# Performance work log

Measured on AMD Instinct MI355X. Metric: run time of the kernel, lower is better.

## Reference

```python
import jax, jax.numpy as jnp
import numpy as np

# tiny-cuda-nn canonical 2D image hash-grid config
L = 16            # n_levels
F = 2             # n_features_per_level
T = 1 << 19       # hashmap size per level
BASE = 16         # base_resolution
SCALE = 1.5       # per_level_scale
HIDDEN = 64
ENC_DIM = L * F   # 32
OUT = 3           # rgb
S = 1024          # img_res / output_size
PRIME_Y = np.uint32(2654435761)


def setup_inputs() -> dict:
    key = jax.random.key(0)
    k1, k2, k3, k4 = jax.random.split(key, 4)
    # pixel-center grid exactly as in the torch module
    half = 0.5 / S
    xs = jnp.linspace(half, 1.0 - half, S, dtype=jnp.float32)
    xv, yv = jnp.meshgrid(xs, xs, indexing='ij')
    xy = jnp.stack([yv.flatten(), xv.flatten()], axis=1)  # [S*S, 2]
    # tcnn initializes hash tables ~ U(-1e-4, 1e-4)
    hash_tables = jax.random.uniform(k1, (L, T, F), jnp.float32, -1e-4, 1e-4)
    W0 = jax.random.normal(k2, (ENC_DIM, HIDDEN), jnp.float32) * np.sqrt(2.0 / ENC_DIM)
    W1 = jax.random.normal(k3, (HIDDEN, HIDDEN), jnp.float32) * np.sqrt(2.0 / HIDDEN)
    W2 = jax.random.normal(k4, (HIDDEN, OUT), jnp.float32) * np.sqrt(2.0 / HIDDEN)
    return {"xy": xy, "hash_tables": hash_tables, "W0": W0, "W1": W1, "W2": W2}


def _encode(xy, hash_tables):
    # multiresolution hash-grid encoding with bilinear interpolation
    resolutions = jnp.floor(BASE * SCALE ** jnp.arange(L)).astype(jnp.int32)  # [L]
    offs = jnp.array([[0, 0], [0, 1], [1, 0], [1, 1]], jnp.int32)            # [4,2]

    def level(table, res):
        pos = xy * res.astype(xy.dtype)            # [N,2]
        p0 = jnp.floor(pos).astype(jnp.int32)
        w = pos - p0                                # frac weights [N,2]
        corners = p0[:, None, :] + offs[None]       # [N,4,2]
        # hashed index (tcnn spatial hash): x*1 ^ y*PRIME, mod T
        cu = corners.astype(jnp.uint32)
        hidx = ((cu[..., 0] ^ (cu[..., 1] * PRIME_Y)) % np.uint32(T)).astype(jnp.int32)
        # dense index when the grid fits in the table
        didx = corners[..., 0] + corners[..., 1] * (res + 1)
        idx = jnp.where((res + 1) * (res + 1) <= T, didx, hidx)  # [N,4]
        f = table[idx]                               # [N,4,F] gather
        wx, wy = w[:, 0:1], w[:, 1:2]
        wts = jnp.stack([(1 - wx) * (1 - wy), (1 - wx) * wy,
                         wx * (1 - wy), wx * wy], axis=1)  # [N,4,1]
        return jnp.sum(f * wts, axis=1)              # [N,F]

    feats = jax.vmap(level, in_axes=(0, 0), out_axes=1)(hash_tables, resolutions)  # [N,L,F]
    return feats.reshape(feats.shape[0], ENC_DIM)


def reference(xy, hash_tables, W0, W1, W2):
    enc = _encode(xy, hash_tables)                  # [N,32]
    h = jax.nn.relu(enc @ W0)                       # tiny MLP, no bias (FullyFusedMLP)
    h = jax.nn.relu(h @ W1)
    out = h @ W2                                    # [N,3], linear output
    return out.reshape(S, S, OUT).transpose(2, 0, 1)  # [3,S,S]
```

## Files before the change

### kernel.cpp

```cpp
#include <hip/hip_runtime.h>
#include <cstdint>
#include <cstddef>

#define S_DIM 1024
#define NPTS (S_DIM * S_DIM)
#define NLEV 16
#define TBL (1u << 19)
#define TMASK (TBL - 1u)
#define PRIME_Y 2654435761u

typedef float v4f __attribute__((ext_vector_type(4)));
typedef short v8s __attribute__((ext_vector_type(8)));

__device__ __forceinline__ void split2(float a, float b, uint32_t& hi, uint32_t& lo) {
    uint32_t ua = __float_as_uint(a), ub = __float_as_uint(b);
    uint32_t ha = ua & 0xFFFF0000u, hb = ub & 0xFFFF0000u;
    float la = a - __uint_as_float(ha);
    float lb = b - __uint_as_float(hb);
    hi = (ha >> 16) | hb;
    lo = (__float_as_uint(la) >> 16) | (__float_as_uint(lb) & 0xFFFF0000u);
}

__global__ __launch_bounds__(256) void prep_weights(const float* __restrict__ W0,
                                                    const float* __restrict__ W1,
                                                    uint4* __restrict__ ws) {
    const int tid = threadIdx.x;
    const int lane = tid & 63;
    const int m = lane & 15, q = lane >> 4;

    {
        const int tile = tid >> 6;
        const int n = tile * 16 + m;
        uint32_t hi[4], lo[4];
        #pragma unroll
        for (int d = 0; d < 4; ++d) {
            const int k0 = q * 8 + 2 * d;
            split2(W0[k0 * 64 + n], W0[(k0 + 1) * 64 + n], hi[d], lo[d]);
        }
        ws[tid]       = make_uint4(hi[0], hi[1], hi[2], hi[3]);
        ws[256 + tid] = make_uint4(lo[0], lo[1], lo[2], lo[3]);
    }

    #pragma unroll
    for (int rep = 0; rep < 2; ++rep) {
        const int unit = tid + rep * 256;
        const int l2 = unit & 63, frag = unit >> 6;
        const int nt = frag >> 1, ks = frag & 1;
        const int mm = l2 & 15, qq = l2 >> 4;
        const int n = nt * 16 + mm;
        uint32_t hi[4], lo[4];
        #pragma unroll
        for (int d = 0; d < 4; ++d) {
            const int k0 = ks * 32 + qq * 8 + 2 * d;
            split2(W1[k0 * 64 + n], W1[(k0 + 1) * 64 + n], hi[d], lo[d]);
        }
        ws[512 + unit]  = make_uint4(hi[0], hi[1], hi[2], hi[3]);
        ws[1024 + unit] = make_uint4(lo[0], lo[1], lo[2], lo[3]);
    }
}

static __device__ __forceinline__ float2 level_feat_rt(float x, float y, float fr,
                                                       int st , bool dense,
                                                       const float* __restrict__ tb) {
    const float px = x * fr, py = y * fr;
    const float fx = floorf(px), fy = floorf(py);
    const float wx = px - fx, wy = py - fy;
    const int x0 = (int)fx, y0 = (int)fy;

    const int d00 = x0 + y0 * st;
    const int d01 = d00 + st;
    const unsigned a = (unsigned)x0, b = (unsigned)y0;
    const unsigned hb0 = b * PRIME_Y;
    const unsigned hb1 = hb0 + PRIME_Y;
    const int h00 = (int)((a ^ hb0) & TMASK);
    const int h01 = (int)((a ^ hb1) & TMASK);
    const int h10 = (int)(((a + 1u) ^ hb0) & TMASK);
    const int h11 = (int)(((a + 1u) ^ hb1) & TMASK);

    const int i00 = dense ? d00 : h00;
    const int i01 = dense ? d01 : h01;
    const int i10 = dense ? (d00 + 1) : h10;
    const int i11 = dense ? (d01 + 1) : h11;

    const float2 f00 = *(const float2*)(tb + 2 * (size_t)i00);
    const float2 f01 = *(const float2*)(tb + 2 * (size_t)i01);
    const float2 f10 = *(const float2*)(tb + 2 * (size_t)i10);
    const float2 f11 = *(const float2*)(tb + 2 * (size_t)i11);

    const float omx = 1.f - wx, omy = 1.f - wy;
    const float w00 = omx * omy, w01 = omx * wy, w10 = wx * omy, w11 = wx * wy;

    float2 e;
    e.x = f00.x * w00 + f01.x * w01 + f10.x * w10 + f11.x * w11;
    e.y = f00.y * w00 + f01.y * w01 + f10.y * w10 + f11.y * w11;
    return e;
}

__global__ __launch_bounds__(256, 2) void ngp_mfma(
    const float* __restrict__ xy,
    const float* __restrict__ tables,
    const float* __restrict__ W2,
    const uint4* __restrict__ ws,
    float* __restrict__ out)
{
    __shared__ uint4 w1LDS[1024];
    __shared__ alignas(16) uint32_t h0LDS[4 * 16 * 68];
    __shared__ alignas(16) float w2t[3 * 64];

    const int tid = threadIdx.x;
    const int lane = tid & 63;
    const int wave = tid >> 6;
    const int m = lane & 15, q = lane >> 4;
    const int blockBase = blockIdx.x * 256;
    const int pbase = blockBase + wave * 64 + m;

    #pragma unroll
    for (int r = 0; r < 4; ++r) w1LDS[r * 256 + tid] = ws[512 + r * 256 + tid];
    if (tid < 192) w2t[(tid % 3) * 64 + (tid / 3)] = W2[tid];

    v8s w0h[4], w0l[4];
    #pragma unroll
    for (int t4 = 0; t4 < 4; ++t4) {
        w0h[t4] = __builtin_bit_cast(v8s, ws[t4 * 64 + lane]);
        w0l[t4] = __builtin_bit_cast(v8s, ws[256 + t4 * 64 + lane]);
    }

    constexpr float RESF[NLEV] = {16.f, 24.f, 36.f, 54.f, 81.f, 121.f, 182.f, 273.f,
                                  410.f, 615.f, 922.f, 1383.f, 2075.f, 3113.f, 4670.f, 7006.f};
#define LVLF(i) ((q & 2) ? ((q & 1) ? RESF[12 + (i)] : RESF[8 + (i)]) \
                         : ((q & 1) ? RESF[4 + (i)]  : RESF[(i)]))
    const float fr0 = LVLF(0), fr1 = LVLF(1), fr2 = LVLF(2), fr3 = LVLF(3);
#undef LVLF
    const int st0 = (int)fr0 + 1, st1 = (int)fr1 + 1;
    const int st2 = (int)fr2 + 1, st3 = (int)fr3 + 1;
    const bool dn0 = (q <= 2), dn1 = (q <= 2), dn2 = (q <= 1), dn3 = (q <= 1);
    const float* tb0 = tables + ((size_t)(unsigned)(q * 4 + 0) << 20);
    const float* tb1 = tables + ((size_t)(unsigned)(q * 4 + 1) << 20);
    const float* tb2 = tables + ((size_t)(unsigned)(q * 4 + 2) << 20);
    const float* tb3 = tables + ((size_t)(unsigned)(q * 4 + 3) << 20);

    __syncthreads();

    #pragma unroll 1
    for (int t = 0; t < 4; ++t) {
        const float2 p = ((const float2*)xy)[pbase + t * 16];
        const float2 e0 = level_feat_rt(p.x, p.y, fr0, st0, dn0, tb0);
        const float2 e1 = level_feat_rt(p.x, p.y, fr1, st1, dn1, tb1);
        const float2 e2 = level_feat_rt(p.x, p.y, fr2, st2, dn2, tb2);
        const float2 e3 = level_feat_rt(p.x, p.y, fr3, st3, dn3, tb3);
        uint32_t eh0, el0, eh1, el1, eh2, el2, eh3, el3;
        split2(e0.x, e0.y, eh0, el0);
        split2(e1.x, e1.y, eh1, el1);
        split2(e2.x, e2.y, eh2, el2);
        split2(e3.x, e3.y, eh3, el3);
        const v8s eH = __builtin_bit_cast(v8s, make_uint4(eh0, eh1, eh2, eh3));
        const v8s eL = __builtin_bit_cast(v8s, make_uint4(el0, el1, el2, el3));

        v4f acc0[4];
        #pragma unroll
        for (int nt = 0; nt < 4; ++nt) {
            v4f c = {0.f, 0.f, 0.f, 0.f};
            c = __builtin_amdgcn_mfma_f32_16x16x32_bf16(w0l[nt], eH, c, 0, 0, 0);
            c = __builtin_amdgcn_mfma_f32_16x16x32_bf16(w0h[nt], eL, c, 0, 0, 0);
            c = __builtin_amdgcn_mfma_f32_16x16x32_bf16(w0h[nt], eH, c, 0, 0, 0);
            acc0[nt] = c;
        }

        uint32_t* hrow = h0LDS + (wave * 16 + m) * 68;
        #pragma unroll
        for (int nt = 0; nt < 4; ++nt) {
            const float r0 = fmaxf(acc0[nt][0], 0.f), r1 = fmaxf(acc0[nt][1], 0.f);
            const float r2 = fmaxf(acc0[nt][2], 0.f), r3 = fmaxf(acc0[nt][3], 0.f);
            uint32_t h0w, l0w, h1w, l1w;
            split2(r0, r1, h0w, l0w);
            split2(r2, r3, h1w, l1w);
            *((uint2*)(hrow + nt * 8 + q * 2))      = make_uint2(h0w, h1w);
            *((uint2*)(hrow + 32 + nt * 8 + q * 2)) = make_uint2(l0w, l1w);
        }

        const v8s b0H = __builtin_bit_cast(v8s, *((const uint4*)(hrow + q * 4)));
        const v8s b0L = __builtin_bit_cast(v8s, *((const uint4*)(hrow + 32 + q * 4)));
        const v8s b1H = __builtin_bit_cast(v8s, *((const uint4*)(hrow + 16 + q * 4)));
        const v8s b1L = __builtin_bit_cast(v8s, *((const uint4*)(hrow + 48 + q * 4)));

        float o0 = 0.f, o1 = 0.f, o2 = 0.f;
        #pragma unroll
        for (int nt = 0; nt < 4; ++nt) {
            const v8s a0h = __builtin_bit_cast(v8s, w1LDS[(nt * 2 + 0) * 64 + lane]);
            const v8s a0l = __builtin_bit_cast(v8s, w1LDS[512 + (nt * 2 + 0) * 64 + lane]);
            const v8s a1h = __builtin_bit_cast(v8s, w1LDS[(nt * 2 + 1) * 64 + lane]);
            const v8s a1l = __builtin_bit_cast(v8s, w1LDS[512 + (nt * 2 + 1) * 64 + lane]);
            v4f c = {0.f, 0.f, 0.f, 0.f};
            c = __builtin_amdgcn_mfma_f32_16x16x32_bf16(a0l, b0H, c, 0, 0, 0);
            c = __builtin_amdgcn_mfma_f32_16x16x32_bf16(a0h, b0L, c, 0, 0, 0);
            c = __builtin_amdgcn_mfma_f32_16x16x32_bf16(a0h, b0H, c, 0, 0, 0);
            c = __builtin_amdgcn_mfma_f32_16x16x32_bf16(a1l, b1H, c, 0, 0, 0);
            c = __builtin_amdgcn_mfma_f32_16x16x32_bf16(a1h, b1L, c, 0, 0, 0);
            c = __builtin_amdgcn_mfma_f32_16x16x32_bf16(a1h, b1H, c, 0, 0, 0);

            const int n = nt * 16 + q * 4;
            const float4 wa = *((const float4*)(w2t + 0 * 64 + n));
            const float4 wb = *((const float4*)(w2t + 1 * 64 + n));
            const float4 wc = *((const float4*)(w2t + 2 * 64 + n));
            const float h0r = fmaxf(c[0], 0.f), h1r = fmaxf(c[1], 0.f);
            const float h2r = fmaxf(c[2], 0.f), h3r = fmaxf(c[3], 0.f);
            o0 = fmaf(h0r, wa.x, fmaf(h1r, wa.y, fmaf(h2r, wa.z, fmaf(h3r, wa.w, o0))));
            o1 = fmaf(h0r, wb.x, fmaf(h1r, wb.y, fmaf(h2r, wb.z, fmaf(h3r, wb.w, o1))));
            o2 = fmaf(h0r, wc.x, fmaf(h1r, wc.y, fmaf(h2r, wc.z, fmaf(h3r, wc.w, o2))));
        }

        o0 += __shfl_xor(o0, 16); o0 += __shfl_xor(o0, 32);
        o1 += __shfl_xor(o1, 16); o1 += __shfl_xor(o1, 32);
        o2 += __shfl_xor(o2, 16); o2 += __shfl_xor(o2, 32);

        if (lane < 16) {
            const int pidx = blockBase + wave * 64 + t * 16 + lane;
            out[pidx] = o0;
            out[NPTS + pidx] = o1;
            out[2 * NPTS + pidx] = o2;
        }
    }
}

extern "C" void kernel_launch(void* const* d_in, const int* in_sizes, int n_in,
                              void* d_out, int out_size, void* d_ws, size_t ws_size,
                              hipStream_t stream) {
    const float* xy     = (const float*)d_in[0];
    const float* tables = (const float*)d_in[1];
    const float* W0     = (const float*)d_in[2];
    const float* W1     = (const float*)d_in[3];
    const float* W2     = (const float*)d_in[4];
    float* out = (float*)d_out;
    uint4* ws  = (uint4*)d_ws;

    hipLaunchKernelGGL(prep_weights, dim3(1), dim3(256), 0, stream, W0, W1, ws);
    hipLaunchKernelGGL(ngp_mfma, dim3(NPTS / 256), dim3(256), 0, stream,
                       xy, tables, W2, ws, out);
}
```

Baseline: 186.5 us.

## Software-pipeline hash-table gathers one tile ahead of the MLP compute

Splits the level lookup into an issue phase (index computation and gathers) and an interpolation phase. The gathers for the next 16-point tile are issued before the current tile's MFMA work, and the first tile's gathers are issued before the weight staging into LDS, so gather latency can hide behind compute. The bilinear interpolation also moves to packed 2-wide FMAs. In exchange, about 40 extra VGPRs hold the in-flight gather results, which may press occupancy at launch bounds of 256 threads with 2 blocks.

```diff
diff --git a/kernel.cpp b/kernel.cpp
--- a/kernel.cpp
+++ b/kernel.cpp
@@ -9,8 +9,14 @@
 #define TMASK (TBL - 1u)
 #define PRIME_Y 2654435761u
 
+typedef float v2f __attribute__((ext_vector_type(2)));
 typedef float v4f __attribute__((ext_vector_type(4)));
 typedef short v8s __attribute__((ext_vector_type(8)));
+
+static __device__ __forceinline__ v2f fma2(v2f a, v2f b, v2f c) {
+    return __builtin_elementwise_fma(a, b, c);
+}
+static __device__ __forceinline__ v2f splat2(float s) { return (v2f){s, s}; }
 
 __device__ __forceinline__ void split2(float a, float b, uint32_t& hi, uint32_t& lo) {
     uint32_t ua = __float_as_uint(a), ub = __float_as_uint(b);
@@ -59,40 +65,36 @@
     }
 }
 
-static __device__ __forceinline__ float2 level_feat_rt(float x, float y, float fr,
-                                                       int st , bool dense,
-                                                       const float* __restrict__ tb) {
+static __device__ __forceinline__ void level_issue(
+    float x, float y, float fr, int st, bool dense, const float* __restrict__ tb,
+    v2f& w, v2f& f00, v2f& f01, v2f& f10, v2f& f11)
+{
     const float px = x * fr, py = y * fr;
     const float fx = floorf(px), fy = floorf(py);
-    const float wx = px - fx, wy = py - fy;
+    w = (v2f){px - fx, py - fy};
     const int x0 = (int)fx, y0 = (int)fy;
 
     const int d00 = x0 + y0 * st;
-    const int d01 = d00 + st;
     const unsigned a = (unsigned)x0, b = (unsigned)y0;
-    const unsigned hb0 = b * PRIME_Y;
-    const unsigned hb1 = hb0 + PRIME_Y;
-    const int h00 = (int)((a ^ hb0) & TMASK);
-    const int h01 = (int)((a ^ hb1) & TMASK);
-    const int h10 = (int)(((a + 1u) ^ hb0) & TMASK);
-    const int h11 = (int)(((a + 1u) ^ hb1) & TMASK);
-
-    const int i00 = dense ? d00 : h00;
-    const int i01 = dense ? d01 : h01;
-    const int i10 = dense ? (d00 + 1) : h10;
-    const int i11 = dense ? (d01 + 1) : h11;
-
-    const float2 f00 = *(const float2*)(tb + 2 * (size_t)i00);
-    const float2 f01 = *(const float2*)(tb + 2 * (size_t)i01);
-    const float2 f10 = *(const float2*)(tb + 2 * (size_t)i10);
-    const float2 f11 = *(const float2*)(tb + 2 * (size_t)i11);
-
-    const float omx = 1.f - wx, omy = 1.f - wy;
-    const float w00 = omx * omy, w01 = omx * wy, w10 = wx * omy, w11 = wx * wy;
-
-    float2 e;
-    e.x = f00.x * w00 + f01.x * w01 + f10.x * w10 + f11.x * w11;
-    e.y = f00.y * w00 + f01.y * w01 + f10.y * w10 + f11.y * w11;
+    const unsigned hb0 = b * PRIME_Y, hb1 = hb0 + PRIME_Y;
+    const int i00 = dense ? d00          : (int)((a ^ hb0) & TMASK);
+    const int i01 = dense ? d00 + st     : (int)((a ^ hb1) & TMASK);
+    const int i10 = dense ? d00 + 1      : (int)(((a + 1u) ^ hb0) & TMASK);
+    const int i11 = dense ? d00 + st + 1 : (int)(((a + 1u) ^ hb1) & TMASK);
+
+    f00 = *(const v2f*)(tb + 2 * (size_t)i00);
+    f01 = *(const v2f*)(tb + 2 * (size_t)i01);
+    f10 = *(const v2f*)(tb + 2 * (size_t)i10);
+    f11 = *(const v2f*)(tb + 2 * (size_t)i11);
+}
+
+static __device__ __forceinline__ v2f interp2(v2f w, v2f f00, v2f f01, v2f f10, v2f f11) {
+    const float omx = 1.f - w.x, omy = 1.f - w.y;
+    const float w00 = omx * omy, w01 = omx * w.y, w10 = w.x * omy, w11 = w.x * w.y;
+    v2f e = f00 * splat2(w00);
+    e = fma2(f01, splat2(w01), e);
+    e = fma2(f10, splat2(w10), e);
+    e = fma2(f11, splat2(w11), e);
     return e;
 }
 
@@ -113,17 +115,6 @@
     const int m = lane & 15, q = lane >> 4;
     const int blockBase = blockIdx.x * 256;
     const int pbase = blockBase + wave * 64 + m;
-
-    #pragma unroll
-    for (int r = 0; r < 4; ++r) w1LDS[r * 256 + tid] = ws[512 + r * 256 + tid];
-    if (tid < 192) w2t[(tid % 3) * 64 + (tid / 3)] = W2[tid];
-
-    v8s w0h[4], w0l[4];
-    #pragma unroll
-    for (int t4 = 0; t4 < 4; ++t4) {
-        w0h[t4] = __builtin_bit_cast(v8s, ws[t4 * 64 + lane]);
-        w0l[t4] = __builtin_bit_cast(v8s, ws[256 + t4 * 64 + lane]);
-    }
 
     constexpr float RESF[NLEV] = {16.f, 24.f, 36.f, 54.f, 81.f, 121.f, 182.f, 273.f,
                                   410.f, 615.f, 922.f, 1383.f, 2075.f, 3113.f, 4670.f, 7006.f};
@@ -139,15 +130,47 @@
     const float* tb2 = tables + ((size_t)(unsigned)(q * 4 + 2) << 20);
     const float* tb3 = tables + ((size_t)(unsigned)(q * 4 + 3) << 20);
 
+    v2f cw0, cw1, cw2, cw3;
+    v2f c0a, c0b, c0c, c0d, c1a, c1b, c1c, c1d;
+    v2f c2a, c2b, c2c, c2d, c3a, c3b, c3c, c3d;
+    {
+        const float2 p = ((const float2*)xy)[pbase];
+        level_issue(p.x, p.y, fr0, st0, dn0, tb0, cw0, c0a, c0b, c0c, c0d);
+        level_issue(p.x, p.y, fr1, st1, dn1, tb1, cw1, c1a, c1b, c1c, c1d);
+        level_issue(p.x, p.y, fr2, st2, dn2, tb2, cw2, c2a, c2b, c2c, c2d);
+        level_issue(p.x, p.y, fr3, st3, dn3, tb3, cw3, c3a, c3b, c3c, c3d);
+    }
+
+    #pragma unroll
+    for (int r = 0; r < 4; ++r) w1LDS[r * 256 + tid] = ws[512 + r * 256 + tid];
+    if (tid < 192) w2t[(tid % 3) * 64 + (tid / 3)] = W2[tid];
+
+    v8s w0h[4], w0l[4];
+    #pragma unroll
+    for (int t4 = 0; t4 < 4; ++t4) {
+        w0h[t4] = __builtin_bit_cast(v8s, ws[t4 * 64 + lane]);
+        w0l[t4] = __builtin_bit_cast(v8s, ws[256 + t4 * 64 + lane]);
+    }
+
     __syncthreads();
 
     #pragma unroll 1
     for (int t = 0; t < 4; ++t) {
-        const float2 p = ((const float2*)xy)[pbase + t * 16];
-        const float2 e0 = level_feat_rt(p.x, p.y, fr0, st0, dn0, tb0);
-        const float2 e1 = level_feat_rt(p.x, p.y, fr1, st1, dn1, tb1);
-        const float2 e2 = level_feat_rt(p.x, p.y, fr2, st2, dn2, tb2);
-        const float2 e3 = level_feat_rt(p.x, p.y, fr3, st3, dn3, tb3);
+        v2f nw0, nw1, nw2, nw3;
+        v2f n0a, n0b, n0c, n0d, n1a, n1b, n1c, n1d;
+        v2f n2a, n2b, n2c, n2d, n3a, n3b, n3c, n3d;
+        if (t < 3) {
+            const float2 pn = ((const float2*)xy)[pbase + (t + 1) * 16];
+            level_issue(pn.x, pn.y, fr0, st0, dn0, tb0, nw0, n0a, n0b, n0c, n0d);
+            level_issue(pn.x, pn.y, fr1, st1, dn1, tb1, nw1, n1a, n1b, n1c, n1d);
+            level_issue(pn.x, pn.y, fr2, st2, dn2, tb2, nw2, n2a, n2b, n2c, n2d);
+            level_issue(pn.x, pn.y, fr3, st3, dn3, tb3, nw3, n3a, n3b, n3c, n3d);
+        }
+
+        const v2f e0 = interp2(cw0, c0a, c0b, c0c, c0d);
+        const v2f e1 = interp2(cw1, c1a, c1b, c1c, c1d);
+        const v2f e2 = interp2(cw2, c2a, c2b, c2c, c2d);
+        const v2f e3 = interp2(cw3, c3a, c3b, c3c, c3d);
         uint32_t eh0, el0, eh1, el1, eh2, el2, eh3, el3;
         split2(e0.x, e0.y, eh0, el0);
         split2(e1.x, e1.y, eh1, el1);
@@ -219,6 +242,14 @@
             out[NPTS + pidx] = o1;
             out[2 * NPTS + pidx] = o2;
         }
+
+        if (t < 3) {
+            cw0 = nw0; cw1 = nw1; cw2 = nw2; cw3 = nw3;
+            c0a = n0a; c0b = n0b; c0c = n0c; c0d = n0d;
+            c1a = n1a; c1b = n1b; c1c = n1c; c1d = n1d;
+            c2a = n2a; c2b = n2b; c2c = n2c; c2d = n2d;
+            c3a = n3a; c3b = n3b; c3c = n3c; c3d = n3d;
+        }
     }
 }
 
```

Result: slower. 235.8 us (+26.4%).

## Split fused kernel into separate hash-encode and MFMA MLP kernels via workspace

Applied to the files above, without the earlier changes.

Replaces the single fused encode+MLP kernel with a dedicated encoding kernel that writes bf16 hi/lo-split features to a workspace buffer, followed by an MLP kernel that reads them and runs the MFMA layers. Each encoding thread handles four levels for one point, and the MLP kernel prefetches the next tile's encoding and reads W2 from a global transposed copy instead of LDS. The aim is to decouple the latency-bound hash gathers from the MFMA work so each kernel can be tuned and occupied independently. The cost is an extra 128 MB write plus read through global memory and an extra launch, and the fused path is kept as a fallback when the workspace is too small.

```diff
diff --git a/kernel.cpp b/kernel.cpp
--- a/kernel.cpp
+++ b/kernel.cpp
@@ -9,8 +9,14 @@
 #define TMASK (TBL - 1u)
 #define PRIME_Y 2654435761u
 
+typedef float v2f __attribute__((ext_vector_type(2)));
 typedef float v4f __attribute__((ext_vector_type(4)));
 typedef short v8s __attribute__((ext_vector_type(8)));
+
+static __device__ __forceinline__ v2f fma2(v2f a, v2f b, v2f c) {
+    return __builtin_elementwise_fma(a, b, c);
+}
+static __device__ __forceinline__ v2f splat2(float s) { return (v2f){s, s}; }
 
 __device__ __forceinline__ void split2(float a, float b, uint32_t& hi, uint32_t& lo) {
     uint32_t ua = __float_as_uint(a), ub = __float_as_uint(b);
@@ -59,6 +65,12 @@
     }
 }
 
+__global__ __launch_bounds__(256) void prep_w2t(const float* __restrict__ W2,
+                                                float* __restrict__ w2tG) {
+    const int tid = threadIdx.x;
+    if (tid < 192) w2tG[(tid % 3) * 64 + (tid / 3)] = W2[tid];
+}
+
 static __device__ __forceinline__ float2 level_feat_rt(float x, float y, float fr,
                                                        int st , bool dense,
                                                        const float* __restrict__ tb) {
@@ -68,19 +80,12 @@
     const int x0 = (int)fx, y0 = (int)fy;
 
     const int d00 = x0 + y0 * st;
-    const int d01 = d00 + st;
     const unsigned a = (unsigned)x0, b = (unsigned)y0;
-    const unsigned hb0 = b * PRIME_Y;
-    const unsigned hb1 = hb0 + PRIME_Y;
-    const int h00 = (int)((a ^ hb0) & TMASK);
-    const int h01 = (int)((a ^ hb1) & TMASK);
-    const int h10 = (int)(((a + 1u) ^ hb0) & TMASK);
-    const int h11 = (int)(((a + 1u) ^ hb1) & TMASK);
-
-    const int i00 = dense ? d00 : h00;
-    const int i01 = dense ? d01 : h01;
-    const int i10 = dense ? (d00 + 1) : h10;
-    const int i11 = dense ? (d01 + 1) : h11;
+    const unsigned hb0 = b * PRIME_Y, hb1 = hb0 + PRIME_Y;
+    const int i00 = dense ? d00          : (int)((a ^ hb0) & TMASK);
+    const int i01 = dense ? d00 + st     : (int)((a ^ hb1) & TMASK);
+    const int i10 = dense ? d00 + 1      : (int)(((a + 1u) ^ hb0) & TMASK);
+    const int i11 = dense ? d00 + st + 1 : (int)(((a + 1u) ^ hb1) & TMASK);
 
     const float2 f00 = *(const float2*)(tb + 2 * (size_t)i00);
     const float2 f01 = *(const float2*)(tb + 2 * (size_t)i01);
@@ -94,6 +99,151 @@
     e.x = f00.x * w00 + f01.x * w01 + f10.x * w10 + f11.x * w11;
     e.y = f00.y * w00 + f01.y * w01 + f10.y * w10 + f11.y * w11;
     return e;
+}
+
+__global__ __launch_bounds__(256) void ngp_encode(
+    const float* __restrict__ xy,
+    const float* __restrict__ tables,
+    uint4* __restrict__ encHi,
+    uint4* __restrict__ encLo)
+{
+    const int tid = threadIdx.x;
+    const int q = tid >> 6;
+    const int pl = tid & 63;
+    const int p = blockIdx.x * 64 + pl;
+
+    constexpr float RESF[NLEV] = {16.f, 24.f, 36.f, 54.f, 81.f, 121.f, 182.f, 273.f,
+                                  410.f, 615.f, 922.f, 1383.f, 2075.f, 3113.f, 4670.f, 7006.f};
+#define LVLF(i) ((q & 2) ? ((q & 1) ? RESF[12 + (i)] : RESF[8 + (i)]) \
+                         : ((q & 1) ? RESF[4 + (i)]  : RESF[(i)]))
+    const float fr0 = LVLF(0), fr1 = LVLF(1), fr2 = LVLF(2), fr3 = LVLF(3);
+#undef LVLF
+    const int st0 = (int)fr0 + 1, st1 = (int)fr1 + 1;
+    const int st2 = (int)fr2 + 1, st3 = (int)fr3 + 1;
+    const bool dn0 = (q <= 2), dn1 = (q <= 2), dn2 = (q <= 1), dn3 = (q <= 1);
+    const float* tb0 = tables + ((size_t)(unsigned)(q * 4 + 0) << 20);
+    const float* tb1 = tables + ((size_t)(unsigned)(q * 4 + 1) << 20);
+    const float* tb2 = tables + ((size_t)(unsigned)(q * 4 + 2) << 20);
+    const float* tb3 = tables + ((size_t)(unsigned)(q * 4 + 3) << 20);
+
+    const float2 pt = ((const float2*)xy)[p];
+    const float2 e0 = level_feat_rt(pt.x, pt.y, fr0, st0, dn0, tb0);
+    const float2 e1 = level_feat_rt(pt.x, pt.y, fr1, st1, dn1, tb1);
+    const float2 e2 = level_feat_rt(pt.x, pt.y, fr2, st2, dn2, tb2);
+    const float2 e3 = level_feat_rt(pt.x, pt.y, fr3, st3, dn3, tb3);
+
+    uint32_t eh0, el0, eh1, el1, eh2, el2, eh3, el3;
+    split2(e0.x, e0.y, eh0, el0);
+    split2(e1.x, e1.y, eh1, el1);
+    split2(e2.x, e2.y, eh2, el2);
+    split2(e3.x, e3.y, eh3, el3);
+
+    const int idx = blockIdx.x * 256 + (pl >> 4) * 64 + q * 16 + (pl & 15);
+    encHi[idx] = make_uint4(eh0, eh1, eh2, eh3);
+    encLo[idx] = make_uint4(el0, el1, el2, el3);
+}
+
+__global__ __launch_bounds__(256, 2) void ngp_mlp(
+    const uint4* __restrict__ ws,
+    const uint4* __restrict__ encHi,
+    const uint4* __restrict__ encLo,
+    const float* __restrict__ w2tG,
+    float* __restrict__ out)
+{
+    __shared__ alignas(16) uint32_t h0LDS[4 * 16 * 68];
+
+    const int tid = threadIdx.x;
+    const int lane = tid & 63;
+    const int wave = tid >> 6;
+    const int m = lane & 15, q = lane >> 4;
+    const int blockBase = blockIdx.x * 256;
+    const int tileBase = blockIdx.x * 16 + wave * 4;
+
+    v8s w0h[4], w0l[4];
+    #pragma unroll
+    for (int t4 = 0; t4 < 4; ++t4) {
+        w0h[t4] = __builtin_bit_cast(v8s, ws[t4 * 64 + lane]);
+        w0l[t4] = __builtin_bit_cast(v8s, ws[256 + t4 * 64 + lane]);
+    }
+
+    uint4 cH = encHi[tileBase * 64 + lane];
+    uint4 cL = encLo[tileBase * 64 + lane];
+
+    #pragma unroll 1
+    for (int t = 0; t < 4; ++t) {
+        const int tn = (t < 3) ? (t + 1) : 3;
+        const uint4 nH = encHi[(tileBase + tn) * 64 + lane];
+        const uint4 nL = encLo[(tileBase + tn) * 64 + lane];
+
+        const v8s eH = __builtin_bit_cast(v8s, cH);
+        const v8s eL = __builtin_bit_cast(v8s, cL);
+
+        v4f acc0[4];
+        #pragma unroll
+        for (int nt = 0; nt < 4; ++nt) {
+            v4f c = {0.f, 0.f, 0.f, 0.f};
+            c = __builtin_amdgcn_mfma_f32_16x16x32_bf16(w0l[nt], eH, c, 0, 0, 0);
+            c = __builtin_amdgcn_mfma_f32_16x16x32_bf16(w0h[nt], eL, c, 0, 0, 0);
+            c = __builtin_amdgcn_mfma_f32_16x16x32_bf16(w0h[nt], eH, c, 0, 0, 0);
+            acc0[nt] = c;
+        }
+
+        uint32_t* hrow = h0LDS + (wave * 16 + m) * 68;
+        #pragma unroll
+        for (int nt = 0; nt < 4; ++nt) {
+            const float r0 = fmaxf(acc0[nt][0], 0.f), r1 = fmaxf(acc0[nt][1], 0.f);
+            const float r2 = fmaxf(acc0[nt][2], 0.f), r3 = fmaxf(acc0[nt][3], 0.f);
+            uint32_t h0w, l0w, h1w, l1w;
+            split2(r0, r1, h0w, l0w);
+            split2(r2, r3, h1w, l1w);
+            *((uint2*)(hrow + nt * 8 + q * 2))      = make_uint2(h0w, h1w);
+            *((uint2*)(hrow + 32 + nt * 8 + q * 2)) = make_uint2(l0w, l1w);
+        }
+
+        const v8s b0H = __builtin_bit_cast(v8s, *((const uint4*)(hrow + q * 4)));
+        const v8s b0L = __builtin_bit_cast(v8s, *((const uint4*)(hrow + 32 + q * 4)));
+        const v8s b1H = __builtin_bit_cast(v8s, *((const uint4*)(hrow + 16 + q * 4)));
+        const v8s b1L = __builtin_bit_cast(v8s, *((const uint4*)(hrow + 48 + q * 4)));
+
+        float o0 = 0.f, o1 = 0.f, o2 = 0.f;
+        #pragma unroll
+        for (int nt = 0; nt < 4; ++nt) {
+            const v8s a0h = __builtin_bit_cast(v8s, ws[512 + (nt * 2 + 0) * 64 + lane]);
+            const v8s a0l = __builtin_bit_cast(v8s, ws[1024 + (nt * 2 + 0) * 64 + lane]);
+            const v8s a1h = __builtin_bit_cast(v8s, ws[512 + (nt * 2 + 1) * 64 + lane]);
+            const v8s a1l = __builtin_bit_cast(v8s, ws[1024 + (nt * 2 + 1) * 64 + lane]);
+            v4f c = {0.f, 0.f, 0.f, 0.f};
+            c = __builtin_amdgcn_mfma_f32_16x16x32_bf16(a0l, b0H, c, 0, 0, 0);
+            c = __builtin_amdgcn_mfma_f32_16x16x32_bf16(a0h, b0L, c, 0, 0, 0);
+            c = __builtin_amdgcn_mfma_f32_16x16x32_bf16(a0h, b0H, c, 0, 0, 0);
+            c = __builtin_amdgcn_mfma_f32_16x16x32_bf16(a1l, b1H, c, 0, 0, 0);
+            c = __builtin_amdgcn_mfma_f32_16x16x32_bf16(a1h, b1L, c, 0, 0, 0);
+            c = __builtin_amdgcn_mfma_f32_16x16x32_bf16(a1h, b1H, c, 0, 0, 0);
+
+            const int n = nt * 16 + q * 4;
+            const float4 wa = *((const float4*)(w2tG + 0 * 64 + n));
+            const float4 wb = *((const float4*)(w2tG + 1 * 64 + n));
+            const float4 wc = *((const float4*)(w2tG + 2 * 64 + n));
+            const float h0r = fmaxf(c[0], 0.f), h1r = fmaxf(c[1], 0.f);
+            const float h2r = fmaxf(c[2], 0.f), h3r = fmaxf(c[3], 0.f);
+            o0 = fmaf(h0r, wa.x, fmaf(h1r, wa.y, fmaf(h2r, wa.z, fmaf(h3r, wa.w, o0))));
+            o1 = fmaf(h0r, wb.x, fmaf(h1r, wb.y, fmaf(h2r, wb.z, fmaf(h3r, wb.w, o1))));
+            o2 = fmaf(h0r, wc.x, fmaf(h1r, wc.y, fmaf(h2r, wc.z, fmaf(h3r, wc.w, o2))));
+        }
+
+        o0 += __shfl_xor(o0, 16); o0 += __shfl_xor(o0, 32);
+        o1 += __shfl_xor(o1, 16); o1 += __shfl_xor(o1, 32);
+        o2 += __shfl_xor(o2, 16); o2 += __shfl_xor(o2, 32);
+
+        if (lane < 16) {
+            const int pidx = blockBase + wave * 64 + t * 16 + lane;
+            out[pidx] = o0;
+            out[NPTS + pidx] = o1;
+            out[2 * NPTS + pidx] = o2;
+        }
+
+        cH = nH; cL = nL;
+    }
 }
 
 __global__ __launch_bounds__(256, 2) void ngp_mfma(
@@ -233,7 +383,21 @@
     float* out = (float*)d_out;
     uint4* ws  = (uint4*)d_ws;
 
+    const size_t NEED = 25344ull + 2ull * 64ull * 1024ull * 1024ull;
+
     hipLaunchKernelGGL(prep_weights, dim3(1), dim3(256), 0, stream, W0, W1, ws);
-    hipLaunchKernelGGL(ngp_mfma, dim3(NPTS / 256), dim3(256), 0, stream,
-                       xy, tables, W2, ws, out);
-}
+
+    if (ws_size >= NEED) {
+        float* w2tG = (float*)((char*)d_ws + 24576);
+        uint4* encHi = (uint4*)((char*)d_ws + 25344);
+        uint4* encLo = encHi + (NPTS / 16) * 64;
+        hipLaunchKernelGGL(prep_w2t, dim3(1), dim3(256), 0, stream, W2, w2tG);
+        hipLaunchKernelGGL(ngp_encode, dim3(NPTS / 64), dim3(256), 0, stream,
+                           xy, tables, encHi, encLo);
+        hipLaunchKernelGGL(ngp_mlp, dim3(NPTS / 256), dim3(256), 0, stream,
+                           ws, encHi, encLo, w2tG, out);
+    } else {
+        hipLaunchKernelGGL(ngp_mfma, dim3(NPTS / 256), dim3(256), 0, stream,
+                           xy, tables, W2, ws, out);
+    }
+}
```

New measurement: 214.8 us. +15.1%, slower.
